# Optimization experiments

Hardware: AMD Instinct MI355X
Metric: run time of the kernel (lower is better)

Reference implementation:

```python
import jax, jax.numpy as jnp
import numpy as np

N_NODES = 100_000
N_EDGES = 3_200_000


def setup_inputs() -> dict:
    key = jax.random.key(0)
    k = jax.random.split(key, 7)
    x = jax.random.normal(k[0], (N_NODES, 1), dtype=jnp.float32)
    edge_index = jax.random.randint(k[1], (2, N_EDGES), 0, N_NODES, dtype=jnp.int64)
    edge_weight = jax.random.uniform(k[2], (N_EDGES,), dtype=jnp.float32)
    # GCNConv params (glorot-style scale)
    W1 = jax.random.normal(k[3], (1, 16), dtype=jnp.float32) * 0.5
    b1 = jnp.zeros((16,), dtype=jnp.float32)
    W2 = jax.random.normal(k[4], (16, 2), dtype=jnp.float32) * 0.25
    b2 = jnp.zeros((2,), dtype=jnp.float32)
    return {"x": x, "edge_index": edge_index, "edge_weight": edge_weight,
            "W1": W1, "b1": b1, "W2": W2, "b2": b2}


def reference(x, edge_index, edge_weight, W1, b1, W2, b2):
    N = x.shape[0]
    src, dst = edge_index[0], edge_index[1]
    # GCN normalization with self-loops (fill value 1.0), cached across both layers
    loop = jnp.arange(N, dtype=edge_index.dtype)
    src_f = jnp.concatenate([src, loop])            # [E+N]
    dst_f = jnp.concatenate([dst, loop])            # [E+N]
    w_f = jnp.concatenate([edge_weight, jnp.ones((N,), dtype=edge_weight.dtype)])
    deg = jax.ops.segment_sum(w_f, dst_f, num_segments=N)   # [N]
    dinv = jnp.where(deg > 0, jax.lax.rsqrt(deg), 0.0)
    norm = dinv[src_f] * w_f * dinv[dst_f]          # [E+N]

    def gcn_layer(h, W, b):
        h = h @ W                                   # [N, F_out]
        msg = norm[:, None] * h[src_f]              # gather + weight  [E+N, F_out]
        agg = jax.ops.segment_sum(msg, dst_f, num_segments=N)  # scatter-add [N, F_out]
        return agg + b

    h = jax.nn.relu(gcn_layer(x, W1, b1))
    # F.dropout(training=self.training): identity at inference (reference is eval mode)
    out = gcn_layer(h, W2, b2)
    return jax.nn.log_softmax(out, axis=1)
```

## Files before the change

### kernel.cpp

```cpp
#include <hip/hip_runtime.h>
#include <math.h>


static constexpr int BLOCK_S   = 512;
static constexpr int EPB       = 4096;
static constexpr int VITERS    = EPB / (BLOCK_S * 4);
static constexpr int CHUNK     = 128;
static constexpr int LOG_CHUNK = 7;
static constexpr int BLOCK_A   = 512;
static constexpr int MAXNB     = 1024;
static constexpr int MAXBLK    = 1024;
static constexpr int TABCAP    = 5120;
static constexpr int PAD       = 5120;
static constexpr unsigned int SENT = 0xFFFFFFFFu;

__device__ __forceinline__ unsigned int incl_scan512(unsigned int v,
                                                     unsigned int* wsum, int t) {
    unsigned int x = v;
#pragma unroll
    for (int off = 1; off < 64; off <<= 1) {
        unsigned int y = __shfl_up(x, off, 64);
        if ((t & 63) >= off) x += y;
    }
    if ((t & 63) == 63) wsum[t >> 6] = x;
    __syncthreads();
    if (t < 8) {
        unsigned int s = wsum[t];
#pragma unroll
        for (int off = 1; off < 8; off <<= 1) {
            unsigned int y = __shfl_up(s, off, 64);
            if (t >= off) s += y;
        }
        wsum[t] = s;
    }
    __syncthreads();
    return x + ((t >= 64) ? wsum[(t >> 6) - 1] : 0u);
}

__device__ __forceinline__ int run_adj_fallback(const unsigned int* cumx,
                                                const int* radj,
                                                unsigned int i, int nblk) {
    int lo = 0, hi = nblk - 1;
    while (lo < hi) {
        int mid = (lo + hi + 1) >> 1;
        if (cumx[mid] <= i) lo = mid; else hi = mid - 1;
    }
    return radj[lo];
}


__global__ __launch_bounds__(BLOCK_S) void scatter_kernel(
    const int* __restrict__ src, const int* __restrict__ dst,
    const float* __restrict__ w,
    unsigned int* __restrict__ rowOffT,
    unsigned long long* __restrict__ payload,
    int E, int nb, int nblk) {
    __shared__ unsigned long long pbuf[EPB];
    __shared__ unsigned int hist[MAXNB];
    __shared__ unsigned int wsum[8];
    const int blk  = blockIdx.x;
    const int base = blk * EPB;
    const int nE   = min(EPB, E - base);
    const int t    = threadIdx.x;

    hist[t]           = 0u;
    hist[t + BLOCK_S] = 0u;
    __syncthreads();

    int4 dc[VITERS];
#pragma unroll
    for (int i = 0; i < VITERS; ++i) {
        const int k = 4 * t + i * 4 * BLOCK_S;
        int4 d4 = make_int4(0, 0, 0, 0);
        if (k < nE) {
            d4 = *reinterpret_cast<const int4*>(&dst[base + k]);
            atomicAdd(&hist[(unsigned int)d4.x >> LOG_CHUNK], 1u);
            atomicAdd(&hist[(unsigned int)d4.y >> LOG_CHUNK], 1u);
            atomicAdd(&hist[(unsigned int)d4.z >> LOG_CHUNK], 1u);
            atomicAdd(&hist[(unsigned int)d4.w >> LOG_CHUNK], 1u);
        }
        dc[i] = d4;
    }
    __syncthreads();

    const unsigned int v0 = hist[2 * t], v1 = hist[2 * t + 1];
    const unsigned int pr = v0 + v1;
    const unsigned int inclp = incl_scan512(pr, wsum, t);
    const unsigned int ex0 = inclp - pr;
    const unsigned int ex1 = ex0 + v0;
    if (2 * t < nb)     rowOffT[(size_t)(2 * t) * nblk + blk]     = ex0;
    if (2 * t + 1 < nb) rowOffT[(size_t)(2 * t + 1) * nblk + blk] = ex1;
    if (t == 0)         rowOffT[(size_t)nb * nblk + blk] = (unsigned int)nE;
    hist[2 * t]     = ex0;
    hist[2 * t + 1] = ex1;
    __syncthreads();

#pragma unroll
    for (int i = 0; i < VITERS; ++i) {
        const int k = 4 * t + i * 4 * BLOCK_S;
        if (k < nE) {
            const int4   d4 = dc[i];
            const int4   s4 = *reinterpret_cast<const int4*>(&src[base + k]);
            const float4 w4 = *reinterpret_cast<const float4*>(&w[base + k]);
#define SCAT_ONE(dd, ss, ww)                                                  \
            {                                                                 \
                const unsigned int slot =                                     \
                    atomicAdd(&hist[(unsigned int)(dd) >> LOG_CHUNK], 1u);    \
                pbuf[slot] =                                                  \
                    ((unsigned long long)__float_as_uint(ww) << 32) |         \
                    ((unsigned int)(ss) << LOG_CHUNK) |                       \
                    (unsigned int)((dd) & (CHUNK - 1));                       \
            }
            SCAT_ONE(d4.x, s4.x, w4.x)
            SCAT_ONE(d4.y, s4.y, w4.y)
            SCAT_ONE(d4.z, s4.z, w4.z)
            SCAT_ONE(d4.w, s4.w, w4.w)
#undef SCAT_ONE
        }
    }
    __syncthreads();
    for (int k2 = t; k2 < (nE >> 1); k2 += BLOCK_S) {
        ulonglong2 v = *reinterpret_cast<const ulonglong2*>(&pbuf[2 * k2]);
        *reinterpret_cast<ulonglong2*>(&payload[(size_t)base + 2 * k2]) = v;
    }
}


#define AGG_PROLOGUE                                                          \
    unsigned int s00 = 0, s01 = 0, len0 = 0, len1 = 0;                        \
    {                                                                         \
        const int e0 = 2 * t, e1 = 2 * t + 1;                                 \
        if (e0 < nblk) {                                                      \
            const uint2 r0 =                                                  \
                *reinterpret_cast<const uint2*>(&rowOffT[(size_t)b * nblk + e0]); \
            const uint2 r1 =                                                  \
                *reinterpret_cast<const uint2*>(&rowOffT[(size_t)(b + 1) * nblk + e0]); \
            s00 = r0.x; s01 = r0.y;                                           \
            len0 = r1.x - r0.x;                                               \
            len1 = (e1 < nblk) ? (r1.y - r0.y) : 0u;                          \
        }                                                                     \
        const unsigned int pr_    = len0 + len1;                              \
        const unsigned int inclp_ = incl_scan512(pr_, wsum, t);               \
        const unsigned int ex0_   = inclp_ - pr_;                             \
        const unsigned int ex1_   = ex0_ + len0;                              \
        if (e0 < nblk) { cumx[e0] = ex0_; radj[e0] = (int)s00 - (int)ex0_ + e0 * EPB; } \
        if (e1 < nblk) { cumx[e1] = ex1_; radj[e1] = (int)s01 - (int)ex1_ + e1 * EPB; } \
        if (t == ((nblk - 1) >> 1)) totsh = inclp_;                           \
        __syncthreads();                                                      \
        const unsigned int total_ = totsh;                                    \
        for (int r = e0; r <= e1 && r < nblk; ++r) {                          \
            const unsigned int beg = cumx[r];                                 \
            const unsigned int end = (r == nblk - 1) ? total_ : cumx[r + 1];  \
            const unsigned int lim = min(end, (unsigned int)TABCAP);          \
            const int a_ = radj[r];                                           \
            for (unsigned int i = beg; i < lim; ++i) table[i] = a_;           \
        }                                                                     \
    }                                                                         \
    __syncthreads();

#define TAB(i) (((i) < (unsigned int)TABCAP) ? table[i]                       \
                                             : run_adj_fallback(cumx, radj, (i), nblk))

__global__ __launch_bounds__(BLOCK_A) void deg_dinv_kernel(
    const unsigned long long* __restrict__ payload,
    unsigned long long* __restrict__ payload2,
    unsigned int* __restrict__ bucketCnt,
    const unsigned int* __restrict__ rowOffT,
    const float* __restrict__ x,
    float* __restrict__ dinv, float* __restrict__ xd,
    int N, int nb, int nblk) {
    __shared__ unsigned int cumx[MAXBLK];
    __shared__ int          radj[MAXBLK];
    __shared__ float        acc[CHUNK];
    __shared__ int          table[TABCAP];
    __shared__ unsigned int wsum[8];
    __shared__ unsigned int totsh;
    const int b = blockIdx.x, t = threadIdx.x;
    if (t < CHUNK) acc[t] = 0.0f;
    AGG_PROLOGUE
    const unsigned int total = totsh;
    const bool canw = (total <= (unsigned int)PAD);
    if (t == 0) bucketCnt[b] = canw ? total : SENT;
    unsigned long long* const p2 = payload2 + (size_t)b * PAD;
    unsigned int i = t;
    for (; i + 3u * BLOCK_A < total; i += 4u * BLOCK_A) {
        const unsigned int i0 = i, i1 = i + BLOCK_A, i2 = i + 2u * BLOCK_A,
                           i3 = i + 3u * BLOCK_A;
        const int a0 = TAB(i0), a1 = TAB(i1), a2 = TAB(i2), a3 = TAB(i3);
        const unsigned long long p0 = payload[(unsigned int)(a0 + (int)i0)];
        const unsigned long long p1 = payload[(unsigned int)(a1 + (int)i1)];
        const unsigned long long p2v = payload[(unsigned int)(a2 + (int)i2)];
        const unsigned long long p3 = payload[(unsigned int)(a3 + (int)i3)];
        if (canw) {
            p2[i0] = p0; p2[i1] = p1; p2[i2] = p2v; p2[i3] = p3;
        }
        atomicAdd(&acc[(unsigned int)p0 & (CHUNK - 1)],
                  __uint_as_float((unsigned int)(p0 >> 32)));
        atomicAdd(&acc[(unsigned int)p1 & (CHUNK - 1)],
                  __uint_as_float((unsigned int)(p1 >> 32)));
        atomicAdd(&acc[(unsigned int)p2v & (CHUNK - 1)],
                  __uint_as_float((unsigned int)(p2v >> 32)));
        atomicAdd(&acc[(unsigned int)p3 & (CHUNK - 1)],
                  __uint_as_float((unsigned int)(p3 >> 32)));
    }
    for (; i < total; i += BLOCK_A) {
        const int adj = TAB(i);
        const unsigned long long p = payload[(unsigned int)(adj + (int)i)];
        if (canw) p2[i] = p;
        atomicAdd(&acc[(unsigned int)p & (CHUNK - 1)],
                  __uint_as_float((unsigned int)(p >> 32)));
    }
    __syncthreads();
    const int n = b * CHUNK + t;
    if (t < CHUNK && n < N) {
        const float d = acc[t] + 1.0f;
        const float r = (d > 0.0f) ? rsqrtf(d) : 0.0f;
        dinv[n] = r;
        xd[n]   = r * x[n];
    }
}


#define FAST_BODY(GATHER_ARR)                                                 \
    const size_t gbase = (size_t)b * PAD;                                     \
    const unsigned int npair = cnt >> 1;                                      \
    unsigned int j = t;                                                       \
    for (; j + 3u * BLOCK_A < npair; j += 4u * BLOCK_A) {                     \
        const ulonglong2 q0 = *reinterpret_cast<const ulonglong2*>(&payload2[gbase + 2u * j]); \
        const ulonglong2 q1 = *reinterpret_cast<const ulonglong2*>(&payload2[gbase + 2u * (j + BLOCK_A)]); \
        const ulonglong2 q2 = *reinterpret_cast<const ulonglong2*>(&payload2[gbase + 2u * (j + 2u * BLOCK_A)]); \
        const ulonglong2 q3 = *reinterpret_cast<const ulonglong2*>(&payload2[gbase + 2u * (j + 3u * BLOCK_A)]); \
        const float f0a = GATHER_ARR[(int)(((unsigned int)q0.x) >> LOG_CHUNK)]; \
        const float f0b = GATHER_ARR[(int)(((unsigned int)q0.y) >> LOG_CHUNK)]; \
        const float f1a = GATHER_ARR[(int)(((unsigned int)q1.x) >> LOG_CHUNK)]; \
        const float f1b = GATHER_ARR[(int)(((unsigned int)q1.y) >> LOG_CHUNK)]; \
        const float f2a = GATHER_ARR[(int)(((unsigned int)q2.x) >> LOG_CHUNK)]; \
        const float f2b = GATHER_ARR[(int)(((unsigned int)q2.y) >> LOG_CHUNK)]; \
        const float f3a = GATHER_ARR[(int)(((unsigned int)q3.x) >> LOG_CHUNK)]; \
        const float f3b = GATHER_ARR[(int)(((unsigned int)q3.y) >> LOG_CHUNK)]; \
        atomicAdd(&acc[(unsigned int)q0.x & (CHUNK - 1)], __uint_as_float((unsigned int)(q0.x >> 32)) * f0a); \
        atomicAdd(&acc[(unsigned int)q0.y & (CHUNK - 1)], __uint_as_float((unsigned int)(q0.y >> 32)) * f0b); \
        atomicAdd(&acc[(unsigned int)q1.x & (CHUNK - 1)], __uint_as_float((unsigned int)(q1.x >> 32)) * f1a); \
        atomicAdd(&acc[(unsigned int)q1.y & (CHUNK - 1)], __uint_as_float((unsigned int)(q1.y >> 32)) * f1b); \
        atomicAdd(&acc[(unsigned int)q2.x & (CHUNK - 1)], __uint_as_float((unsigned int)(q2.x >> 32)) * f2a); \
        atomicAdd(&acc[(unsigned int)q2.y & (CHUNK - 1)], __uint_as_float((unsigned int)(q2.y >> 32)) * f2b); \
        atomicAdd(&acc[(unsigned int)q3.x & (CHUNK - 1)], __uint_as_float((unsigned int)(q3.x >> 32)) * f3a); \
        atomicAdd(&acc[(unsigned int)q3.y & (CHUNK - 1)], __uint_as_float((unsigned int)(q3.y >> 32)) * f3b); \
    }                                                                         \
    for (; j < npair; j += BLOCK_A) {                                         \
        const ulonglong2 q = *reinterpret_cast<const ulonglong2*>(&payload2[gbase + 2u * j]); \
        const float fa = GATHER_ARR[(int)(((unsigned int)q.x) >> LOG_CHUNK)]; \
        const float fb = GATHER_ARR[(int)(((unsigned int)q.y) >> LOG_CHUNK)]; \
        atomicAdd(&acc[(unsigned int)q.x & (CHUNK - 1)], __uint_as_float((unsigned int)(q.x >> 32)) * fa); \
        atomicAdd(&acc[(unsigned int)q.y & (CHUNK - 1)], __uint_as_float((unsigned int)(q.y >> 32)) * fb); \
    }                                                                         \
    if ((cnt & 1u) && t == 0) {                                               \
        const unsigned long long q = payload2[gbase + cnt - 1u];              \
        atomicAdd(&acc[(unsigned int)q & (CHUNK - 1)],                        \
                  __uint_as_float((unsigned int)(q >> 32)) *                  \
                      GATHER_ARR[(int)(((unsigned int)q) >> LOG_CHUNK)]);     \
    }

#define FB_BODY(GATHER_ARR)                                                   \
    AGG_PROLOGUE                                                              \
    const unsigned int total = totsh;                                         \
    for (unsigned int i = t; i < total; i += BLOCK_A) {                       \
        const int adj = TAB(i);                                               \
        const unsigned long long p = payload[(unsigned int)(adj + (int)i)];   \
        atomicAdd(&acc[(unsigned int)p & (CHUNK - 1)],                        \
                  __uint_as_float((unsigned int)(p >> 32)) *                  \
                      GATHER_ARR[(int)(((unsigned int)p) >> LOG_CHUNK)]);     \
    }

__global__ __launch_bounds__(BLOCK_A) void s_gamma_kernel(
    const unsigned long long* __restrict__ payload,
    const unsigned long long* __restrict__ payload2,
    const unsigned int* __restrict__ bucketCnt,
    const unsigned int* __restrict__ rowOffT,
    const float* __restrict__ dinv,
    const float* __restrict__ xd,
    const float* __restrict__ W1,
    const float* __restrict__ b1,
    const float* __restrict__ W2,
    float* __restrict__ gd, int N, int nb, int nblk) {
    __shared__ unsigned int cumx[MAXBLK];
    __shared__ int          radj[MAXBLK];
    __shared__ float        acc[CHUNK];
    __shared__ int          table[TABCAP];
    __shared__ unsigned int wsum[8];
    __shared__ unsigned int totsh;
    const int b = blockIdx.x, t = threadIdx.x;
    const unsigned int cnt = bucketCnt[b];
    if (t < CHUNK) acc[t] = 0.0f;
    __syncthreads();
    if (cnt != SENT) {
        FAST_BODY(xd)
    } else {
        FB_BODY(xd)
    }
    __syncthreads();
    const int n = b * CHUNK + t;
    if (t < CHUNK && n < N) {
        const float dv = dinv[n];
        const float sv = dv * (acc[t] + xd[n]);
        float g = 0.0f;
#pragma unroll
        for (int f = 0; f < 16; ++f) {
            const float h = fmaxf(sv * W1[f] + b1[f], 0.0f);
            g += h * (W2[2 * f + 1] - W2[2 * f + 0]);
        }
        gd[n] = dv * g;
    }
}

__global__ __launch_bounds__(BLOCK_A) void d_out_kernel(
    const unsigned long long* __restrict__ payload,
    const unsigned long long* __restrict__ payload2,
    const unsigned int* __restrict__ bucketCnt,
    const unsigned int* __restrict__ rowOffT,
    const float* __restrict__ dinv,
    const float* __restrict__ gd,
    const float* __restrict__ b2,
    float* __restrict__ out, int N, int nb, int nblk) {
    __shared__ unsigned int cumx[MAXBLK];
    __shared__ int          radj[MAXBLK];
    __shared__ float        acc[CHUNK];
    __shared__ int          table[TABCAP];
    __shared__ unsigned int wsum[8];
    __shared__ unsigned int totsh;
    const int b = blockIdx.x, t = threadIdx.x;
    const unsigned int cnt = bucketCnt[b];
    if (t < CHUNK) acc[t] = 0.0f;
    __syncthreads();
    if (cnt != SENT) {
        FAST_BODY(gd)
    } else {
        FB_BODY(gd)
    }
    __syncthreads();
    const int n = b * CHUNK + t;
    if (t < CHUNK && n < N) {
        const float dv = dinv[n];
        const float d = dv * (acc[t] + gd[n]) + (b2[1] - b2[0]);
        const float lse = fmaxf(d, 0.0f) + log1pf(expf(-fabsf(d)));
        out[2 * n + 0] = -lse;
        out[2 * n + 1] = d - lse;
    }
}


static constexpr int BLOCK = 256;

__global__ void zero_kernel(float* __restrict__ a, float* __restrict__ b, int n2) {
    int i = blockIdx.x * blockDim.x + threadIdx.x;
    if (i < n2) { a[i] = 0.0f; b[i] = 0.0f; }
}
__global__ void deg_kernel(const int* __restrict__ dst, const float* __restrict__ w,
                           float* __restrict__ deg, int E) {
    int e = blockIdx.x * blockDim.x + threadIdx.x;
    if (e < E) atomicAdd(&deg[dst[e]], w[e]);
}
__global__ void dinv_kernel(float* __restrict__ deg, int N) {
    int n = blockIdx.x * blockDim.x + threadIdx.x;
    if (n < N) {
        float d = deg[n] + 1.0f;
        deg[n] = (d > 0.0f) ? rsqrtf(d) : 0.0f;
    }
}
__global__ void s_kernel(const int* __restrict__ src, const int* __restrict__ dst,
                         const float* __restrict__ w, const float* __restrict__ dinv,
                         const float* __restrict__ x, float* __restrict__ s, int E) {
    int e = blockIdx.x * blockDim.x + threadIdx.x;
    if (e < E) {
        int si = src[e], di = dst[e];
        atomicAdd(&s[di], dinv[si] * w[e] * dinv[di] * x[si]);
    }
}
__global__ void g_kernel(const float* __restrict__ s, const float* __restrict__ dinv,
                         const float* __restrict__ x, const float* __restrict__ W1,
                         const float* __restrict__ b1, const float* __restrict__ W2,
                         float2* __restrict__ g, int N) {
    int n = blockIdx.x * blockDim.x + threadIdx.x;
    if (n < N) {
        float dv = dinv[n];
        float sv = s[n] + dv * dv * x[n];
        float g0 = 0.0f, g1 = 0.0f;
#pragma unroll
        for (int f = 0; f < 16; ++f) {
            float h = fmaxf(sv * W1[f] + b1[f], 0.0f);
            g0 += h * W2[2 * f + 0];
            g1 += h * W2[2 * f + 1];
        }
        g[n] = make_float2(g0, g1);
    }
}
__global__ void agg2_kernel(const int* __restrict__ src, const int* __restrict__ dst,
                            const float* __restrict__ w, const float* __restrict__ dinv,
                            const float2* __restrict__ g, float* __restrict__ agg, int E) {
    int e = blockIdx.x * blockDim.x + threadIdx.x;
    if (e < E) {
        int si = src[e], di = dst[e];
        float norm = dinv[si] * w[e] * dinv[di];
        float2 gv = g[si];
        atomicAdd(&agg[2 * di + 0], norm * gv.x);
        atomicAdd(&agg[2 * di + 1], norm * gv.y);
    }
}
__global__ void out_kernel(float* __restrict__ out, const float* __restrict__ dinv,
                           const float2* __restrict__ g, const float* __restrict__ b2, int N) {
    int n = blockIdx.x * blockDim.x + threadIdx.x;
    if (n < N) {
        float dv2 = dinv[n] * dinv[n];
        float2 gv = g[n];
        float a0 = out[2 * n + 0] + dv2 * gv.x + b2[0];
        float a1 = out[2 * n + 1] + dv2 * gv.y + b2[1];
        float m = fmaxf(a0, a1);
        float lse = m + logf(expf(a0 - m) + expf(a1 - m));
        out[2 * n + 0] = a0 - lse;
        out[2 * n + 1] = a1 - lse;
    }
}


extern "C" void kernel_launch(void* const* d_in, const int* in_sizes, int n_in,
                              void* d_out, int out_size, void* d_ws, size_t ws_size,
                              hipStream_t stream) {
    const float* x  = (const float*)d_in[0];
    const int*   ei = (const int*)d_in[1];
    const float* w  = (const float*)d_in[2];
    const float* W1 = (const float*)d_in[3];
    const float* b1 = (const float*)d_in[4];
    const float* W2 = (const float*)d_in[5];
    const float* b2 = (const float*)d_in[6];
    float* out = (float*)d_out;

    const int N = in_sizes[0];
    const int E = in_sizes[2];
    const int* src = ei;
    const int* dst = ei + E;

    const int nb   = (N + CHUNK - 1) / CHUNK;
    const int nblk = (E + EPB - 1) / EPB;

    size_t off = 0;
    size_t payload_off  = off;  off += (size_t)nblk * EPB * 8;
    size_t payload2_off = off;  off += (size_t)nb * PAD * 8;
    size_t rowoff_off   = off;  off += (size_t)(nb + 1) * nblk * 4 + 8;
    off = (off + 7) & ~(size_t)7;
    size_t bcnt_off     = off;  off += (size_t)nb * 4;
    size_t dinv_off     = off;  off += (size_t)N * 4;
    size_t xd_off       = off;  off += (size_t)N * 4;
    size_t gd_off       = off;  off += (size_t)N * 4;
    const size_t required = off;

    const bool fits = (nb <= MAXNB && nb <= 2 * BLOCK_S && nblk <= MAXBLK &&
                       nblk <= 2 * BLOCK_A && (nblk & 1) == 0 && (E % 4) == 0 &&
                       ws_size >= required);

    if (fits) {
        char* wsb = (char*)d_ws;
        unsigned long long* payload  = (unsigned long long*)(wsb + payload_off);
        unsigned long long* payload2 = (unsigned long long*)(wsb + payload2_off);
        unsigned int* rowOffT   = (unsigned int*)(wsb + rowoff_off);
        unsigned int* bucketCnt = (unsigned int*)(wsb + bcnt_off);
        float* dinv = (float*)(wsb + dinv_off);
        float* xd   = (float*)(wsb + xd_off);
        float* gd   = (float*)(wsb + gd_off);

        scatter_kernel <<<nblk, BLOCK_S, 0, stream>>>(src, dst, w, rowOffT, payload,
                                                      E, nb, nblk);
        deg_dinv_kernel<<<nb, BLOCK_A, 0, stream>>>(payload, payload2, bucketCnt,
                                                    rowOffT, x, dinv, xd, N, nb, nblk);
        s_gamma_kernel <<<nb, BLOCK_A, 0, stream>>>(payload, payload2, bucketCnt,
                                                    rowOffT, dinv, xd,
                                                    W1, b1, W2, gd, N, nb, nblk);
        d_out_kernel   <<<nb, BLOCK_A, 0, stream>>>(payload, payload2, bucketCnt,
                                                    rowOffT, dinv, gd, b2,
                                                    out, N, nb, nblk);
    } else {
        float*  ws   = (float*)d_ws;
        float*  dinv = ws;
        float*  s    = ws + (size_t)N;
        float2* g    = (float2*)(ws + (size_t)2 * N);
        const int gridE  = (E + BLOCK - 1) / BLOCK;
        const int gridN  = (N + BLOCK - 1) / BLOCK;
        const int gridN2 = (2 * N + BLOCK - 1) / BLOCK;
        zero_kernel<<<gridN2, BLOCK, 0, stream>>>(ws, out, 2 * N);
        deg_kernel <<<gridE,  BLOCK, 0, stream>>>(dst, w, dinv, E);
        dinv_kernel<<<gridN,  BLOCK, 0, stream>>>(dinv, N);
        s_kernel   <<<gridE,  BLOCK, 0, stream>>>(src, dst, w, dinv, x, s, E);
        g_kernel   <<<gridN,  BLOCK, 0, stream>>>(s, dinv, x, W1, b1, W2, g, N);
        agg2_kernel<<<gridE,  BLOCK, 0, stream>>>(src, dst, w, dinv, g, out, E);
        out_kernel <<<gridN,  BLOCK, 0, stream>>>(out, dinv, g, b2, N);
    }
}
```

Before: 182.8 us.

## Double node bucket width to 256 and use 1024-thread aggregation blocks

Node buckets grow from 128 to 256 destinations and aggregation blocks grow to 1024 threads, so each thread handles one bucket or source block in the scans instead of two. This halves the number of buckets and aggregation blocks, which means fewer per-block prologue scans and fewer rowOffT rows to read. The s_gamma and d_out kernels drop the shared run-adjust table and fall back to a binary search per edge. Larger buckets double the padded payload2 and table sizes, raising shared memory use and possibly lowering occupancy.

```diff
diff --git a/kernel.cpp b/kernel.cpp
--- a/kernel.cpp
+++ b/kernel.cpp
@@ -5,13 +5,13 @@
 static constexpr int BLOCK_S   = 512;
 static constexpr int EPB       = 4096;
 static constexpr int VITERS    = EPB / (BLOCK_S * 4);
-static constexpr int CHUNK     = 128;
-static constexpr int LOG_CHUNK = 7;
-static constexpr int BLOCK_A   = 512;
-static constexpr int MAXNB     = 1024;
+static constexpr int CHUNK     = 256;
+static constexpr int LOG_CHUNK = 8;
+static constexpr int BLOCK_A   = 1024;
+static constexpr int MAXNB     = 512;
 static constexpr int MAXBLK    = 1024;
-static constexpr int TABCAP    = 5120;
-static constexpr int PAD       = 5120;
+static constexpr int TABCAP    = 10240;
+static constexpr int PAD       = 10240;
 static constexpr unsigned int SENT = 0xFFFFFFFFu;
 
 __device__ __forceinline__ unsigned int incl_scan512(unsigned int v,
@@ -28,6 +28,29 @@
         unsigned int s = wsum[t];
 #pragma unroll
         for (int off = 1; off < 8; off <<= 1) {
+            unsigned int y = __shfl_up(s, off, 64);
+            if (t >= off) s += y;
+        }
+        wsum[t] = s;
+    }
+    __syncthreads();
+    return x + ((t >= 64) ? wsum[(t >> 6) - 1] : 0u);
+}
+
+__device__ __forceinline__ unsigned int incl_scan1024(unsigned int v,
+                                                      unsigned int* wsum, int t) {
+    unsigned int x = v;
+#pragma unroll
+    for (int off = 1; off < 64; off <<= 1) {
+        unsigned int y = __shfl_up(x, off, 64);
+        if ((t & 63) >= off) x += y;
+    }
+    if ((t & 63) == 63) wsum[t >> 6] = x;
+    __syncthreads();
+    if (t < 16) {
+        unsigned int s = wsum[t];
+#pragma unroll
+        for (int off = 1; off < 16; off <<= 1) {
             unsigned int y = __shfl_up(s, off, 64);
             if (t >= off) s += y;
         }
@@ -47,7 +70,6 @@
     }
     return radj[lo];
 }
-
 
 __global__ __launch_bounds__(BLOCK_S) void scatter_kernel(
     const int* __restrict__ src, const int* __restrict__ dst,
@@ -63,8 +85,7 @@
     const int nE   = min(EPB, E - base);
     const int t    = threadIdx.x;
 
-    hist[t]           = 0u;
-    hist[t + BLOCK_S] = 0u;
+    hist[t] = 0u;
     __syncthreads();
 
     int4 dc[VITERS];
@@ -83,16 +104,12 @@
     }
     __syncthreads();
 
-    const unsigned int v0 = hist[2 * t], v1 = hist[2 * t + 1];
-    const unsigned int pr = v0 + v1;
-    const unsigned int inclp = incl_scan512(pr, wsum, t);
-    const unsigned int ex0 = inclp - pr;
-    const unsigned int ex1 = ex0 + v0;
-    if (2 * t < nb)     rowOffT[(size_t)(2 * t) * nblk + blk]     = ex0;
-    if (2 * t + 1 < nb) rowOffT[(size_t)(2 * t + 1) * nblk + blk] = ex1;
-    if (t == 0)         rowOffT[(size_t)nb * nblk + blk] = (unsigned int)nE;
-    hist[2 * t]     = ex0;
-    hist[2 * t + 1] = ex1;
+    const unsigned int val  = hist[t];
+    const unsigned int incl = incl_scan512(val, wsum, t);
+    const unsigned int excl = incl - val;
+    if (t < nb)  rowOffT[(size_t)t * nblk + blk]  = excl;
+    if (t == 0)  rowOffT[(size_t)nb * nblk + blk] = (unsigned int)nE;
+    hist[t] = excl;
     __syncthreads();
 
 #pragma unroll
@@ -125,42 +142,6 @@
     }
 }
 
-
-#define AGG_PROLOGUE                                                          \
-    unsigned int s00 = 0, s01 = 0, len0 = 0, len1 = 0;                        \
-    {                                                                         \
-        const int e0 = 2 * t, e1 = 2 * t + 1;                                 \
-        if (e0 < nblk) {                                                      \
-            const uint2 r0 =                                                  \
-                *reinterpret_cast<const uint2*>(&rowOffT[(size_t)b * nblk + e0]); \
-            const uint2 r1 =                                                  \
-                *reinterpret_cast<const uint2*>(&rowOffT[(size_t)(b + 1) * nblk + e0]); \
-            s00 = r0.x; s01 = r0.y;                                           \
-            len0 = r1.x - r0.x;                                               \
-            len1 = (e1 < nblk) ? (r1.y - r0.y) : 0u;                          \
-        }                                                                     \
-        const unsigned int pr_    = len0 + len1;                              \
-        const unsigned int inclp_ = incl_scan512(pr_, wsum, t);               \
-        const unsigned int ex0_   = inclp_ - pr_;                             \
-        const unsigned int ex1_   = ex0_ + len0;                              \
-        if (e0 < nblk) { cumx[e0] = ex0_; radj[e0] = (int)s00 - (int)ex0_ + e0 * EPB; } \
-        if (e1 < nblk) { cumx[e1] = ex1_; radj[e1] = (int)s01 - (int)ex1_ + e1 * EPB; } \
-        if (t == ((nblk - 1) >> 1)) totsh = inclp_;                           \
-        __syncthreads();                                                      \
-        const unsigned int total_ = totsh;                                    \
-        for (int r = e0; r <= e1 && r < nblk; ++r) {                          \
-            const unsigned int beg = cumx[r];                                 \
-            const unsigned int end = (r == nblk - 1) ? total_ : cumx[r + 1];  \
-            const unsigned int lim = min(end, (unsigned int)TABCAP);          \
-            const int a_ = radj[r];                                           \
-            for (unsigned int i = beg; i < lim; ++i) table[i] = a_;           \
-        }                                                                     \
-    }                                                                         \
-    __syncthreads();
-
-#define TAB(i) (((i) < (unsigned int)TABCAP) ? table[i]                       \
-                                             : run_adj_fallback(cumx, radj, (i), nblk))
-
 __global__ __launch_bounds__(BLOCK_A) void deg_dinv_kernel(
     const unsigned long long* __restrict__ payload,
     unsigned long long* __restrict__ payload2,
@@ -173,14 +154,35 @@
     __shared__ int          radj[MAXBLK];
     __shared__ float        acc[CHUNK];
     __shared__ int          table[TABCAP];
-    __shared__ unsigned int wsum[8];
+    __shared__ unsigned int wsum[16];
     __shared__ unsigned int totsh;
     const int b = blockIdx.x, t = threadIdx.x;
     if (t < CHUNK) acc[t] = 0.0f;
-    AGG_PROLOGUE
+
+    unsigned int s0 = 0, len = 0;
+    if (t < nblk) {
+        s0  = rowOffT[(size_t)b * nblk + t];
+        len = rowOffT[(size_t)(b + 1) * nblk + t] - s0;
+    }
+    const unsigned int incl = incl_scan1024(len, wsum, t);
+    const unsigned int ex   = incl - len;
+    if (t < nblk) { cumx[t] = ex; radj[t] = (int)s0 - (int)ex + t * EPB; }
+    if (t == nblk - 1) totsh = incl;
+    __syncthreads();
     const unsigned int total = totsh;
     const bool canw = (total <= (unsigned int)PAD);
     if (t == 0) bucketCnt[b] = canw ? total : SENT;
+    if (t < nblk) {
+        const unsigned int beg = cumx[t];
+        const unsigned int end = (t == nblk - 1) ? total : cumx[t + 1];
+        const unsigned int lim = min(end, (unsigned int)TABCAP);
+        const int a_ = radj[t];
+        for (unsigned int i = beg; i < lim; ++i) table[i] = a_;
+    }
+    __syncthreads();
+
+#define TAB(i) (((i) < (unsigned int)TABCAP) ? table[i]                       \
+                                             : run_adj_fallback(cumx, radj, (i), nblk))
     unsigned long long* const p2 = payload2 + (size_t)b * PAD;
     unsigned int i = t;
     for (; i + 3u * BLOCK_A < total; i += 4u * BLOCK_A) {
@@ -191,9 +193,7 @@
         const unsigned long long p1 = payload[(unsigned int)(a1 + (int)i1)];
         const unsigned long long p2v = payload[(unsigned int)(a2 + (int)i2)];
         const unsigned long long p3 = payload[(unsigned int)(a3 + (int)i3)];
-        if (canw) {
-            p2[i0] = p0; p2[i1] = p1; p2[i2] = p2v; p2[i3] = p3;
-        }
+        if (canw) { p2[i0] = p0; p2[i1] = p1; p2[i2] = p2v; p2[i3] = p3; }
         atomicAdd(&acc[(unsigned int)p0 & (CHUNK - 1)],
                   __uint_as_float((unsigned int)(p0 >> 32)));
         atomicAdd(&acc[(unsigned int)p1 & (CHUNK - 1)],
@@ -210,6 +210,7 @@
         atomicAdd(&acc[(unsigned int)p & (CHUNK - 1)],
                   __uint_as_float((unsigned int)(p >> 32)));
     }
+#undef TAB
     __syncthreads();
     const int n = b * CHUNK + t;
     if (t < CHUNK && n < N) {
@@ -262,14 +263,25 @@
     }
 
 #define FB_BODY(GATHER_ARR)                                                   \
-    AGG_PROLOGUE                                                              \
-    const unsigned int total = totsh;                                         \
-    for (unsigned int i = t; i < total; i += BLOCK_A) {                       \
-        const int adj = TAB(i);                                               \
-        const unsigned long long p = payload[(unsigned int)(adj + (int)i)];   \
-        atomicAdd(&acc[(unsigned int)p & (CHUNK - 1)],                        \
-                  __uint_as_float((unsigned int)(p >> 32)) *                  \
-                      GATHER_ARR[(int)(((unsigned int)p) >> LOG_CHUNK)]);     \
+    {                                                                         \
+        unsigned int s0 = 0, len = 0;                                         \
+        if (t < nblk) {                                                       \
+            s0  = rowOffT[(size_t)b * nblk + t];                              \
+            len = rowOffT[(size_t)(b + 1) * nblk + t] - s0;                   \
+        }                                                                     \
+        const unsigned int incl = incl_scan1024(len, wsum, t);                \
+        const unsigned int ex   = incl - len;                                 \
+        if (t < nblk) { cumx[t] = ex; radj[t] = (int)s0 - (int)ex + t * EPB; } \
+        if (t == nblk - 1) totsh = incl;                                      \
+        __syncthreads();                                                      \
+        const unsigned int total = totsh;                                     \
+        for (unsigned int i = t; i < total; i += BLOCK_A) {                   \
+            const int adj = run_adj_fallback(cumx, radj, i, nblk);            \
+            const unsigned long long p = payload[(unsigned int)(adj + (int)i)]; \
+            atomicAdd(&acc[(unsigned int)p & (CHUNK - 1)],                    \
+                      __uint_as_float((unsigned int)(p >> 32)) *              \
+                          GATHER_ARR[(int)(((unsigned int)p) >> LOG_CHUNK)]); \
+        }                                                                     \
     }
 
 __global__ __launch_bounds__(BLOCK_A) void s_gamma_kernel(
@@ -286,8 +298,7 @@
     __shared__ unsigned int cumx[MAXBLK];
     __shared__ int          radj[MAXBLK];
     __shared__ float        acc[CHUNK];
-    __shared__ int          table[TABCAP];
-    __shared__ unsigned int wsum[8];
+    __shared__ unsigned int wsum[16];
     __shared__ unsigned int totsh;
     const int b = blockIdx.x, t = threadIdx.x;
     const unsigned int cnt = bucketCnt[b];
@@ -325,8 +336,7 @@
     __shared__ unsigned int cumx[MAXBLK];
     __shared__ int          radj[MAXBLK];
     __shared__ float        acc[CHUNK];
-    __shared__ int          table[TABCAP];
-    __shared__ unsigned int wsum[8];
+    __shared__ unsigned int wsum[16];
     __shared__ unsigned int totsh;
     const int b = blockIdx.x, t = threadIdx.x;
     const unsigned int cnt = bucketCnt[b];
@@ -443,19 +453,18 @@
     const int nblk = (E + EPB - 1) / EPB;
 
     size_t off = 0;
-    size_t payload_off  = off;  off += (size_t)nblk * EPB * 8;
-    size_t payload2_off = off;  off += (size_t)nb * PAD * 8;
-    size_t rowoff_off   = off;  off += (size_t)(nb + 1) * nblk * 4 + 8;
-    off = (off + 7) & ~(size_t)7;
-    size_t bcnt_off     = off;  off += (size_t)nb * 4;
-    size_t dinv_off     = off;  off += (size_t)N * 4;
-    size_t xd_off       = off;  off += (size_t)N * 4;
-    size_t gd_off       = off;  off += (size_t)N * 4;
+    auto align16 = [](size_t v) { return (v + 15) & ~(size_t)15; };
+    size_t payload_off  = off;  off = align16(off + (size_t)nblk * EPB * 8);
+    size_t payload2_off = off;  off = align16(off + (size_t)nb * PAD * 8);
+    size_t rowoff_off   = off;  off = align16(off + (size_t)(nb + 1) * nblk * 4);
+    size_t bcnt_off     = off;  off = align16(off + (size_t)nb * 4);
+    size_t dinv_off     = off;  off = align16(off + (size_t)N * 4);
+    size_t xd_off       = off;  off = align16(off + (size_t)N * 4);
+    size_t gd_off       = off;  off = align16(off + (size_t)N * 4);
     const size_t required = off;
 
-    const bool fits = (nb <= MAXNB && nb <= 2 * BLOCK_S && nblk <= MAXBLK &&
-                       nblk <= 2 * BLOCK_A && (nblk & 1) == 0 && (E % 4) == 0 &&
-                       ws_size >= required);
+    const bool fits = (nb <= MAXNB && nb <= BLOCK_S && nblk <= MAXBLK &&
+                       nblk <= BLOCK_A && (E % 4) == 0 && ws_size >= required);
 
     if (fits) {
         char* wsb = (char*)d_ws;
```

After: 178.7 us. 1.02x faster.
